# Optimization experiments

Hardware: AMD Instinct MI355X
Metric: run time of the kernel (lower is better)

Reference implementation:

```python
import jax, jax.numpy as jnp
import numpy as np

BS, DEC, IN_LEN, HID, EMB, VOCAB = 16, 100, 512, 768, 768, 32000


def setup_inputs() -> dict:
    key = jax.random.key(0)
    ks = jax.random.split(key, 8)
    x = jax.random.normal(ks[0], (BS, DEC, HID), dtype=jnp.float32)
    attn_dist = jax.random.normal(ks[1], (BS, DEC, IN_LEN), dtype=jnp.float32)
    enc_input = jax.random.randint(ks[2], (BS, IN_LEN), 0, VOCAB, dtype=jnp.int32)
    enc_output = jax.random.normal(ks[3], (BS, IN_LEN, EMB), dtype=jnp.float32)
    # learned params
    W_vocab = jax.random.normal(ks[4], (HID, VOCAB), dtype=jnp.float32) / np.sqrt(HID)
    b_vocab = jnp.zeros((VOCAB,), dtype=jnp.float32)
    W_gen = jax.random.normal(ks[5], (HID + EMB, 1), dtype=jnp.float32) / np.sqrt(HID + EMB)
    b_gen = jnp.zeros((1,), dtype=jnp.float32)
    return {"x": x, "attn_dist": attn_dist, "enc_input": enc_input,
            "enc_output": enc_output, "W_vocab": W_vocab, "b_vocab": b_vocab,
            "W_gen": W_gen, "b_gen": b_gen}


def reference(x, attn_dist, enc_input, enc_output, W_vocab, b_vocab, W_gen, b_gen):
    # context vector: [bs, dec, emb] = attn @ enc_output
    context = jnp.einsum('bdl,ble->bde', attn_dist, enc_output)
    mix = jnp.concatenate([context, x], axis=2)              # [bs, dec, emb+hid]
    p_gen = jax.nn.sigmoid(mix @ W_gen + b_gen)              # [bs, dec, 1]
    logit = x @ W_vocab + b_vocab                            # [bs, dec, vocab]
    vocab_dist = jax.nn.softmax(logit, axis=2) * p_gen       # [bs, dec, vocab]
    attn_w = jax.nn.softmax(attn_dist, axis=2) * (1.0 - p_gen)  # [bs, dec, in_len]
    # scatter_add attention mass onto vocab ids (duplicate ids accumulate)
    b_idx = jnp.arange(BS)[:, None, None]
    d_idx = jnp.arange(DEC)[None, :, None]
    v_idx = enc_input[:, None, :]                            # broadcast over dec
    mixed = vocab_dist.at[b_idx, d_idx, v_idx].add(attn_w)
    return jnp.log(mixed)
```

## Files before the change

### kernel.cpp

```cpp
#include <hip/hip_runtime.h>
#include <math.h>

#define BS 16
#define DEC 100
#define IN_LEN 512
#define HID 768
#define EMB 768
#define VOCAB 32000
#define NROW (BS*DEC)
#define NTILE_M 13
#define NTILE_N2 125
#define KT2 24
#define A_SHORTS 4096
#define B_SHORTS 8192

using short8 = __attribute__((ext_vector_type(8))) short;
using f32x4 = __attribute__((ext_vector_type(4))) float;

__device__ __forceinline__ unsigned short f2bf(float f) {
  unsigned u = __float_as_uint(f);
  u = u + 0x7FFFu + ((u >> 16) & 1u);
  return (unsigned short)(u >> 16);
}
__device__ __forceinline__ float bf2f(unsigned short h) {
  return __uint_as_float(((unsigned)h) << 16);
}

__device__ __forceinline__ void gll16(const void* g, void* l) {
  __builtin_amdgcn_global_load_lds(
      (const __attribute__((address_space(1))) unsigned int*)g,
      (__attribute__((address_space(3))) unsigned int*)l, 16, 0, 0);
}

__global__ __launch_bounds__(256) void k0_venc(const float* __restrict__ enc_out,
                                               const float* __restrict__ Wg,
                                               float* __restrict__ venc) {
  int row = blockIdx.x * 4 + (threadIdx.x >> 6);
  int lane = threadIdx.x & 63;
  const float* p = enc_out + (size_t)row * EMB;
  float s = 0.f;
  for (int e = lane; e < EMB; e += 64) s += p[e] * Wg[e];
  for (int off = 32; off; off >>= 1) s += __shfl_xor(s, off);
  if (lane == 0) venc[row] = s;
}

__global__ __launch_bounds__(256) void k1_row(const float* __restrict__ attn,
                                              const float* __restrict__ x,
                                              const float* __restrict__ venc,
                                              const float* __restrict__ Wg,
                                              const float* __restrict__ bgen,
                                              float* __restrict__ pg,
                                              float* __restrict__ lp,
                                              float* __restrict__ m_a,
                                              float* __restrict__ s_a) {
  int r = blockIdx.x;
  int b = r / DEC;
  int tid = threadIdx.x;
  const float* arow = attn + (size_t)r * IN_LEN;
  const float* ve = venc + b * IN_LEN;
  const float* xrow = x + (size_t)r * HID;

  float pdot = 0.f, m = -1e30f;
  for (int l = tid; l < IN_LEN; l += 256) { float a = arow[l]; pdot += a * ve[l]; m = fmaxf(m, a); }
  for (int h = tid; h < HID; h += 256) pdot += xrow[h] * Wg[HID + h];

  for (int off = 32; off; off >>= 1) pdot += __shfl_xor(pdot, off);
  for (int off = 32; off; off >>= 1) m = fmaxf(m, __shfl_xor(m, off));

  __shared__ float red[8];
  if ((tid & 63) == 0) { red[tid >> 6] = pdot; red[4 + (tid >> 6)] = m; }
  __syncthreads();
  float z = red[0] + red[1] + red[2] + red[3];
  m = fmaxf(fmaxf(red[4], red[5]), fmaxf(red[6], red[7]));

  float se = 0.f;
  for (int l = tid; l < IN_LEN; l += 256) se += expf(arow[l] - m);
  for (int off = 32; off; off >>= 1) se += __shfl_xor(se, off);
  __syncthreads();
  if ((tid & 63) == 0) red[tid >> 6] = se;
  __syncthreads();
  se = red[0] + red[1] + red[2] + red[3];

  if (tid == 0) {
    z += bgen[0];
    float p, l_p;
    if (z >= 0.f) { float e = expf(-z); p = 1.f / (1.f + e); l_p = -log1pf(e); }
    else          { float e = expf(z);  p = e / (1.f + e);   l_p = z - log1pf(e); }
    pg[r] = p; lp[r] = l_p; m_a[r] = m; s_a[r] = se;
  }
}

__global__ __launch_bounds__(256) void p0_pack_x(const float* __restrict__ X,
                                                 unsigned short* __restrict__ Xp) {
  int mtile = blockIdx.x, ks = blockIdx.y, tid = threadIdx.x;
  size_t base = ((size_t)(mtile * KT2 + ks)) * A_SHORTS;
#pragma unroll
  for (int i = 0; i < 2; i++) {
    int u = tid + i * 256;
    int f = u >> 6, l = u & 63;
    int wr = f >> 2, mm = f & 3;
    int row = mtile * 128 + wr * 64 + mm * 16 + (l & 15);
    int k0 = ks * 32 + (l >> 4) * 8;
    short8 v;
    if (row < NROW) {
      const float* p = X + (size_t)row * HID + k0;
#pragma unroll
      for (int j = 0; j < 8; j++) v[j] = (short)f2bf(p[j]);
    } else {
#pragma unroll
      for (int j = 0; j < 8; j++) v[j] = 0;
    }
    *(short8*)&Xp[base + (size_t)u * 8] = v;
  }
}

__global__ __launch_bounds__(256) void p0_pack_w(const float* __restrict__ W,
                                                 unsigned short* __restrict__ Wp) {
  __shared__ float ld[32][257];
  int ntile = blockIdx.x, ks = blockIdx.y, tid = threadIdx.x;
#pragma unroll
  for (int i = 0; i < 32; i++) {
    int idx = tid + i * 256;
    int kk = idx >> 8, nn = idx & 255;
    ld[kk][nn] = W[(size_t)(ks * 32 + kk) * VOCAB + ntile * 256 + nn];
  }
  __syncthreads();
  size_t base = ((size_t)(ntile * KT2 + ks)) * B_SHORTS;
#pragma unroll
  for (int i = 0; i < 4; i++) {
    int u = tid + i * 256;
    int f = u >> 6, l = u & 63;
    int wc, nn;
    if (f < 8) { wc = f >> 2; nn = f & 3; }
    else       { wc = (f - 8) >> 2; nn = 4 + ((f - 8) & 3); }
    int col = wc * 128 + nn * 16 + (l & 15);
    int k0 = (l >> 4) * 8;
    short8 v;
#pragma unroll
    for (int j = 0; j < 8; j++) v[j] = (short)f2bf(ld[k0 + j][col]);
    *(short8*)&Wp[base + (size_t)u * 8] = v;
  }
}

__global__ __launch_bounds__(256, 2) void k2_gemm_v6(const unsigned short* __restrict__ Xp,
                                                     const unsigned short* __restrict__ Wp,
                                                     const float* __restrict__ bvocab,
                                                     float* __restrict__ out,
                                                     unsigned short* __restrict__ lbf,
                                                     float* __restrict__ part,
                                                     int use_bf) {
  __shared__ __align__(16) unsigned short sh[33792];

  int bid = blockIdx.x;
  const int NWG = NTILE_M * NTILE_N2;
  const int q = NWG / 8, rr = NWG % 8;
  int xcd = bid & 7, idx = bid >> 3;
  int wg = (xcd < rr ? xcd * (q + 1) : rr * (q + 1) + (xcd - rr) * q) + idx;
  int ntile = wg / NTILE_M, mtile = wg % NTILE_M;

  const int tid = threadIdx.x;
  const int wid = tid >> 6, lane = tid & 63;
  const int wr = wid >> 1, wc = wid & 1;
  const int l15 = lane & 15, hi = lane >> 4;

  const unsigned short* aSrc = Xp + (size_t)(mtile * KT2) * A_SHORTS;
  const unsigned short* bSrc = Wp + (size_t)(ntile * KT2) * B_SHORTS;
  const unsigned short* bDir = bSrc + (8 + wc * 4) * 512 + lane * 8;

  unsigned short* bufA0 = &sh[0];
  unsigned short* bufA1 = &sh[4096];
  unsigned short* bufB0 = &sh[8192];
  unsigned short* bufB1 = &sh[12288];

  const int aoff = (wr * 4) * 512 + lane * 8;
  const int boff = (wc * 4) * 512 + lane * 8;

  f32x4 acc[4][8] = {};
  short8 af[4], bl[4], rbA[4], rbB[4];

#define STAGE(t, dA, dB) { \
    const unsigned short* a_ = aSrc + (size_t)(t) * A_SHORTS; \
    const unsigned short* b_ = bSrc + (size_t)(t) * B_SHORTS; \
    gll16(a_ + (size_t)tid * 8,         dA + tid * 8); \
    gll16(a_ + (size_t)(tid + 256) * 8, dA + (tid + 256) * 8); \
    gll16(b_ + (size_t)tid * 8,         dB + tid * 8); \
    gll16(b_ + (size_t)(tid + 256) * 8, dB + (tid + 256) * 8); }

#define LOADDIR(dst, t) { \
    const unsigned short* p_ = bDir + (size_t)(t) * B_SHORTS; \
    _Pragma("unroll") for (int nn = 0; nn < 4; nn++) dst[nn] = *(const short8*)(p_ + nn * 512); }

#define DSREAD(bA, bB) { \
    _Pragma("unroll") for (int mm = 0; mm < 4; mm++) af[mm] = *(const short8*)&bA[aoff + mm * 512]; \
    _Pragma("unroll") for (int nn = 0; nn < 4; nn++) bl[nn] = *(const short8*)&bB[boff + nn * 512]; }

#define MFMA32(rb) { \
    _Pragma("unroll") for (int mm = 0; mm < 4; mm++) { \
      _Pragma("unroll") for (int nn = 0; nn < 4; nn++) \
        acc[mm][nn] = __builtin_amdgcn_mfma_f32_16x16x32_bf16(af[mm], bl[nn], acc[mm][nn], 0, 0, 0); \
      _Pragma("unroll") for (int nn = 0; nn < 4; nn++) \
        acc[mm][4 + nn] = __builtin_amdgcn_mfma_f32_16x16x32_bf16(af[mm], rb[nn], acc[mm][4 + nn], 0, 0, 0); } }

  STAGE(0, bufA0, bufB0);
  LOADDIR(rbA, 0);
  asm volatile("s_waitcnt vmcnt(4)" ::: "memory");
  __builtin_amdgcn_s_barrier();
  asm volatile("" ::: "memory");

  for (int tt = 0; tt < 22; tt += 2) {
    STAGE(tt + 1, bufA1, bufB1);
    LOADDIR(rbB, tt + 1);
    DSREAD(bufA0, bufB0);
    __builtin_amdgcn_s_setprio(1);
    MFMA32(rbA);
    __builtin_amdgcn_s_setprio(0);
    asm volatile("s_waitcnt vmcnt(4)" ::: "memory");
    __builtin_amdgcn_s_barrier();
    asm volatile("" ::: "memory");
    STAGE(tt + 2, bufA0, bufB0);
    LOADDIR(rbA, tt + 2);
    DSREAD(bufA1, bufB1);
    __builtin_amdgcn_s_setprio(1);
    MFMA32(rbB);
    __builtin_amdgcn_s_setprio(0);
    asm volatile("s_waitcnt vmcnt(4)" ::: "memory");
    __builtin_amdgcn_s_barrier();
    asm volatile("" ::: "memory");
  }
  STAGE(23, bufA1, bufB1);
  LOADDIR(rbB, 23);
  DSREAD(bufA0, bufB0);
  __builtin_amdgcn_s_setprio(1);
  MFMA32(rbA);
  __builtin_amdgcn_s_setprio(0);
  asm volatile("s_waitcnt vmcnt(4)" ::: "memory");
  __builtin_amdgcn_s_barrier();
  asm volatile("" ::: "memory");
  DSREAD(bufA1, bufB1);
  MFMA32(rbB);
#undef STAGE
#undef LOADDIR
#undef DSREAD
#undef MFMA32

  __syncthreads();

  float bb[8];
#pragma unroll
  for (int nn = 0; nn < 8; nn++) bb[nn] = bvocab[ntile * 256 + wc * 128 + nn * 16 + l15];
#pragma unroll
  for (int mm = 0; mm < 4; mm++)
#pragma unroll
    for (int nn = 0; nn < 8; nn++)
#pragma unroll
      for (int j = 0; j < 4; j++) acc[mm][nn][j] += bb[nn];

  unsigned short* ldsC = &sh[0];
  float* red = (float*)&sh[32768];

  if (use_bf) {
#pragma unroll
    for (int mm = 0; mm < 4; mm++) {
      int row0 = wr * 64 + mm * 16 + hi * 4;
#pragma unroll
      for (int nn = 0; nn < 8; nn++) {
        int col = wc * 128 + nn * 16 + l15;
#pragma unroll
        for (int j = 0; j < 4; j++) ldsC[(row0 + j) * 256 + col] = f2bf(acc[mm][nn][j]);
      }
    }
  } else {
#pragma unroll
    for (int mm = 0; mm < 4; mm++) {
      int row0 = mtile * 128 + wr * 64 + mm * 16 + hi * 4;
#pragma unroll
      for (int nn = 0; nn < 8; nn++) {
        int col = ntile * 256 + wc * 128 + nn * 16 + l15;
#pragma unroll
        for (int j = 0; j < 4; j++) {
          int row = row0 + j;
          if (row < NROW) out[(size_t)row * VOCAB + col] = acc[mm][nn][j];
        }
      }
    }
  }

#pragma unroll
  for (int mm = 0; mm < 4; mm++) {
#pragma unroll
    for (int j = 0; j < 4; j++) {
      float mx = acc[mm][0][j];
#pragma unroll
      for (int nn = 1; nn < 8; nn++) mx = fmaxf(mx, acc[mm][nn][j]);
      mx = fmaxf(mx, __shfl_xor(mx, 1));
      mx = fmaxf(mx, __shfl_xor(mx, 2));
      mx = fmaxf(mx, __shfl_xor(mx, 4));
      mx = fmaxf(mx, __shfl_xor(mx, 8));
      float sl = 0.f;
#pragma unroll
      for (int nn = 0; nn < 8; nn++) sl += __expf(acc[mm][nn][j] - mx);
      sl += __shfl_xor(sl, 1);
      sl += __shfl_xor(sl, 2);
      sl += __shfl_xor(sl, 4);
      sl += __shfl_xor(sl, 8);
      if (l15 == 0) {
        int rloc = wr * 64 + mm * 16 + hi * 4 + j;
        int o = (rloc * 2 + wc) * 2;
        red[o] = mx; red[o + 1] = sl;
      }
    }
  }
  __syncthreads();

  if (use_bf) {
#pragma unroll
    for (int i = 0; i < 16; i++) {
      int flat = tid + i * 256;
      int r = flat >> 5, c = (flat & 31) * 8;
      int grow = mtile * 128 + r;
      if (grow < NROW)
        *(short8*)&lbf[(size_t)grow * VOCAB + ntile * 256 + c] = *(const short8*)&ldsC[r * 256 + c];
    }
  }
  if (tid < 128) {
    int o0 = (tid * 2 + 0) * 2;
    int o1 = (tid * 2 + 1) * 2;
    float m0 = red[o0], s0 = red[o0 + 1];
    float m1 = red[o1], s1 = red[o1 + 1];
    float m = fmaxf(m0, m1);
    float s = s0 * __expf(m0 - m) + s1 * __expf(m1 - m);
    int grow = mtile * 128 + tid;
    if (grow < NROW) {
      part[(size_t)grow * 256 + ntile * 2]     = m;
      part[(size_t)grow * 256 + ntile * 2 + 1] = s;
    }
  }
}

__global__ __launch_bounds__(512) void k4_fused(float* __restrict__ out,
                                                const unsigned short* __restrict__ lbf,
                                                const float* __restrict__ part,
                                                const float* __restrict__ lp,
                                                const float* __restrict__ attn,
                                                const int* __restrict__ enc,
                                                const float* __restrict__ pg,
                                                const float* __restrict__ m_a,
                                                const float* __restrict__ s_a) {
  int r = blockIdx.x >> 1;
  int half = blockIdx.x & 1;
  int tid = threadIdx.x;
  __shared__ float sm[8], ss[8], sc[1];
  __shared__ int   s_key[1024];
  __shared__ float s_val[1024];
  s_key[tid] = -1; s_key[tid + 512] = -1;
  s_val[tid] = 0.f; s_val[tid + 512] = 0.f;

  float m = -1e30f, s = 0.f;
  if (tid < NTILE_N2) {
    m = part[(size_t)r * 256 + tid * 2];
    s = part[(size_t)r * 256 + tid * 2 + 1];
  }
  for (int off = 1; off < 64; off <<= 1) {
    float mo = __shfl_xor(m, off), so = __shfl_xor(s, off);
    float nm = fmaxf(m, mo);
    s = s * __expf(m - nm) + so * __expf(mo - nm);
    m = nm;
  }
  if ((tid & 63) == 0) { sm[tid >> 6] = m; ss[tid >> 6] = s; }
  __syncthreads();
  if (tid == 0) {
    float mm_ = sm[0], ss_ = ss[0];
    for (int w = 1; w < 8; w++) {
      float nm = fmaxf(mm_, sm[w]);
      ss_ = ss_ * __expf(mm_ - nm) + ss[w] * __expf(sm[w] - nm);
      mm_ = nm;
    }
    sc[0] = lp[r] - (mm_ + __logf(ss_));
  }

  float omp = 1.f - pg[r];
  if (omp > 0.f) {
    int b_ = r / DEC;
    float t = omp * __expf(attn[(size_t)r * IN_LEN + tid] - m_a[r]) / s_a[r];
    int v = enc[b_ * IN_LEN + tid];
    int slot = v & 1023;
    while (true) {
      int old = atomicCAS(&s_key[slot], -1, v);
      if (old == -1 || old == v) { atomicAdd(&s_val[slot], t); break; }
      slot = (slot + 1) & 1023;
    }
  }
  __syncthreads();
  float coef = sc[0];

  const int HUNITS = (VOCAB / 8) / 2;
  const short8* src = (const short8*)(lbf + (size_t)r * VOCAB) + (size_t)half * HUNITS;
  float* dst = out + (size_t)r * VOCAB;
  float* dsth = dst + (size_t)half * (VOCAB / 2);
  for (int i = tid; i < HUNITS; i += 512) {
    short8 v = src[i];
    f32x4 a, b;
    a[0] = bf2f((unsigned short)v[0]) + coef; a[1] = bf2f((unsigned short)v[1]) + coef;
    a[2] = bf2f((unsigned short)v[2]) + coef; a[3] = bf2f((unsigned short)v[3]) + coef;
    b[0] = bf2f((unsigned short)v[4]) + coef; b[1] = bf2f((unsigned short)v[5]) + coef;
    b[2] = bf2f((unsigned short)v[6]) + coef; b[3] = bf2f((unsigned short)v[7]) + coef;
    __builtin_nontemporal_store(a, (f32x4*)&dsth[i * 8]);
    __builtin_nontemporal_store(b, (f32x4*)&dsth[i * 8 + 4]);
  }
  __syncthreads();

  int lo = half * (VOCAB / 2), hiR = lo + (VOCAB / 2);
  for (int i = tid; i < 1024; i += 512) {
    int v = s_key[i];
    if (v >= lo && v < hiR) {
      float sum = s_val[i];
      float p = dst[v];
      dst[v] = logf(expf(p) + sum);
    }
  }
}

__global__ __launch_bounds__(256) void k4_finish(float* __restrict__ out,
                                                 const float* __restrict__ part,
                                                 const float* __restrict__ lp) {
  int r = blockIdx.x >> 1, half = blockIdx.x & 1;
  int tid = threadIdx.x;
  float m = -1e30f, s = 0.f;
  if (tid < NTILE_N2) {
    m = part[(size_t)r * 256 + tid * 2];
    s = part[(size_t)r * 256 + tid * 2 + 1];
  }
  for (int off = 1; off < 64; off <<= 1) {
    float mo = __shfl_xor(m, off), so = __shfl_xor(s, off);
    float nm = fmaxf(m, mo);
    s = s * __expf(m - nm) + so * __expf(mo - nm);
    m = nm;
  }
  __shared__ float sm[4], ss[4], sc[1];
  if ((tid & 63) == 0) { sm[tid >> 6] = m; ss[tid >> 6] = s; }
  __syncthreads();
  if (tid == 0) {
    float mm_ = sm[0], ss_ = ss[0];
    for (int w = 1; w < 4; w++) {
      float nm = fmaxf(mm_, sm[w]);
      ss_ = ss_ * __expf(mm_ - nm) + ss[w] * __expf(sm[w] - nm);
      mm_ = nm;
    }
    sc[0] = lp[r] - (mm_ + __logf(ss_));
  }
  __syncthreads();
  float coef = sc[0];
  float4* p = (float4*)(out + (size_t)r * VOCAB + half * (VOCAB / 2));
  for (int i = tid; i < VOCAB / 8; i += 256) {
    float4 v = p[i];
    v.x += coef; v.y += coef; v.z += coef; v.w += coef;
    p[i] = v;
  }
}

__global__ __launch_bounds__(256) void k4_scatter(float* __restrict__ out,
                                                  const float* __restrict__ attn,
                                                  const int* __restrict__ enc,
                                                  const float* __restrict__ pg,
                                                  const float* __restrict__ m_a,
                                                  const float* __restrict__ s_a) {
  int idx = blockIdx.x * 256 + threadIdx.x;
  int l = idx & (IN_LEN - 1);
  int r = idx >> 9;
  int b = r / DEC;
  float omp = 1.f - pg[r];
  if (omp <= 0.f) return;
  float term = omp * expf(attn[(size_t)r * IN_LEN + l] - m_a[r]) / s_a[r];
  int v = enc[b * IN_LEN + l];
  unsigned* ua = (unsigned*)(out + (size_t)r * VOCAB + v);
  unsigned old = *ua;
  while (true) {
    float f = __uint_as_float(old);
    float nf = logf(expf(f) + term);
    unsigned assumed = old;
    old = atomicCAS(ua, assumed, __float_as_uint(nf));
    if (old == assumed) break;
  }
}

#define BM 128
#define BN 128
#define BK 32
__device__ __forceinline__ int swz_old(int row, int k) {
  int slot = (k >> 3) ^ ((row >> 1) & 3);
  return row * 32 + slot * 8 + (k & 7);
}

__global__ __launch_bounds__(256) void k2_gemm_old(const float* __restrict__ X,
                                                   const float* __restrict__ W,
                                                   const float* __restrict__ bvocab,
                                                   float* __restrict__ out) {
  __shared__ __align__(16) unsigned short As[BM * BK];
  __shared__ __align__(16) unsigned short Bs[BN * BK];
  const int mtile = blockIdx.x;
  const int ntile = blockIdx.y;
  const int tid = threadIdx.x;
  const int wid = tid >> 6, lane = tid & 63;
  const int wr = wid >> 1, wc = wid & 1;
  f32x4 acc[4][4] = {};
  float4 areg[4];
  float  breg[16];
  const int nl = tid & 127;
  const int kg = tid >> 7;
  {
#pragma unroll
    for (int i = 0; i < 4; i++) {
      int idx = tid + i * 256;
      int r = mtile * BM + (idx >> 3);
      if (r < NROW) areg[i] = *(const float4*)(X + (size_t)r * HID + (idx & 7) * 4);
      else areg[i] = make_float4(0.f, 0.f, 0.f, 0.f);
    }
    const float* base = W + (size_t)(kg * 16) * VOCAB + ntile * BN + nl;
#pragma unroll
    for (int i = 0; i < 16; i++) breg[i] = base[(size_t)i * VOCAB];
  }
  const int KS = HID / BK;
  for (int ks = 0; ks < KS; ++ks) {
#pragma unroll
    for (int i = 0; i < 4; i++) {
      int idx = tid + i * 256;
      int r = idx >> 3, kq = idx & 7;
      unsigned short w0 = f2bf(areg[i].x), w1 = f2bf(areg[i].y);
      unsigned short w2 = f2bf(areg[i].z), w3 = f2bf(areg[i].w);
      unsigned short* dstp = &As[swz_old(r, kq * 4)];
      dstp[0] = w0; dstp[1] = w1; dstp[2] = w2; dstp[3] = w3;
    }
    {
      short8 v0, v1;
#pragma unroll
      for (int i = 0; i < 8; i++) { v0[i] = (short)f2bf(breg[i]); v1[i] = (short)f2bf(breg[8 + i]); }
      *(short8*)&Bs[swz_old(nl, kg * 16)] = v0;
      *(short8*)&Bs[swz_old(nl, kg * 16 + 8)] = v1;
    }
    __syncthreads();
    if (ks + 1 < KS) {
      const int ksn = ks + 1;
#pragma unroll
      for (int i = 0; i < 4; i++) {
        int idx = tid + i * 256;
        int r = mtile * BM + (idx >> 3);
        if (r < NROW) areg[i] = *(const float4*)(X + (size_t)r * HID + ksn * BK + (idx & 7) * 4);
        else areg[i] = make_float4(0.f, 0.f, 0.f, 0.f);
      }
      const float* base = W + (size_t)(ksn * BK + kg * 16) * VOCAB + ntile * BN + nl;
#pragma unroll
      for (int i = 0; i < 16; i++) breg[i] = base[(size_t)i * VOCAB];
    }
    {
      const int k0 = (lane >> 4) * 8;
      const int rbase = wr * 64 + (lane & 15);
      const int cbase = wc * 64 + (lane & 15);
      short8 af[4], bf[4];
#pragma unroll
      for (int mm = 0; mm < 4; mm++) af[mm] = *(const short8*)&As[swz_old(rbase + mm * 16, k0)];
#pragma unroll
      for (int nn = 0; nn < 4; nn++) bf[nn] = *(const short8*)&Bs[swz_old(cbase + nn * 16, k0)];
#pragma unroll
      for (int mm = 0; mm < 4; mm++)
#pragma unroll
        for (int nn = 0; nn < 4; nn++)
          acc[mm][nn] = __builtin_amdgcn_mfma_f32_16x16x32_bf16(af[mm], bf[nn], acc[mm][nn], 0, 0, 0);
    }
    __syncthreads();
  }
#pragma unroll
  for (int mm = 0; mm < 4; mm++) {
    int row0 = mtile * BM + wr * 64 + mm * 16 + (lane >> 4) * 4;
#pragma unroll
    for (int nn = 0; nn < 4; nn++) {
      int col = ntile * BN + wc * 64 + nn * 16 + (lane & 15);
      float bb = bvocab[col];
#pragma unroll
      for (int j = 0; j < 4; j++) {
        int row = row0 + j;
        if (row < NROW) out[(size_t)row * VOCAB + col] = acc[mm][nn][j] + bb;
      }
    }
  }
}

__global__ __launch_bounds__(256) void k3_norm(float* __restrict__ out,
                                               const float* __restrict__ lp) {
  int r = blockIdx.x;
  float4* row = reinterpret_cast<float4*>(out + (size_t)r * VOCAB);
  int tid = threadIdx.x;
  float m = -1e30f, s = 0.f;
  for (int i = tid; i < VOCAB / 4; i += 256) {
    float4 v = row[i];
    float m4 = fmaxf(fmaxf(v.x, v.y), fmaxf(v.z, v.w));
    if (m4 > m) { s *= __expf(m - m4); m = m4; }
    s += __expf(v.x - m) + __expf(v.y - m) + __expf(v.z - m) + __expf(v.w - m);
  }
  for (int off = 32; off; off >>= 1) {
    float mo = __shfl_xor(m, off), so = __shfl_xor(s, off);
    float nm = fmaxf(m, mo);
    s = s * __expf(m - nm) + so * __expf(mo - nm);
    m = nm;
  }
  __shared__ float mred[4], sred[4];
  if ((tid & 63) == 0) { mred[tid >> 6] = m; sred[tid >> 6] = s; }
  __syncthreads();
  if (tid == 0) {
    float mm = mred[0], ss = sred[0];
    for (int w = 1; w < 4; w++) {
      float mo = mred[w], so = sred[w];
      float nm = fmaxf(mm, mo);
      ss = ss * __expf(mm - nm) + so * __expf(mo - nm);
      mm = nm;
    }
    mred[0] = mm; sred[0] = ss;
  }
  __syncthreads();
  m = mred[0]; s = sred[0];
  float coef = lp[r] - (m + __logf(s));
  for (int i = tid; i < VOCAB / 4; i += 256) {
    float4 v = row[i];
    v.x += coef; v.y += coef; v.z += coef; v.w += coef;
    row[i] = v;
  }
}

extern "C" void kernel_launch(void* const* d_in, const int* in_sizes, int n_in,
                              void* d_out, int out_size, void* d_ws, size_t ws_size,
                              hipStream_t stream) {
  (void)in_sizes; (void)n_in; (void)out_size;
  const float* x       = (const float*)d_in[0];
  const float* attn    = (const float*)d_in[1];
  const int*   enc_in  = (const int*)d_in[2];
  const float* enc_out = (const float*)d_in[3];
  const float* Wv      = (const float*)d_in[4];
  const float* bv      = (const float*)d_in[5];
  const float* Wg      = (const float*)d_in[6];
  const float* bg      = (const float*)d_in[7];
  float* out = (float*)d_out;
  float* ws  = (float*)d_ws;

  float* venc = ws;
  float* pg   = ws + 8192;
  float* lp   = ws + 9792;
  float* m_a  = ws + 11392;
  float* s_a  = ws + 12992;
  float* part = ws + 14592;
  unsigned short* Xp = (unsigned short*)(ws + 814592);
  unsigned short* Wp = (unsigned short*)(ws + 1453568);
  unsigned short* Lbf = (unsigned short*)(ws + 13741568);
  const size_t NEED  = (size_t)13741568 * 4;
  const size_t NEED2 = NEED + (size_t)NROW * VOCAB * 2;

  hipLaunchKernelGGL(k0_venc, dim3(2048), dim3(256), 0, stream, enc_out, Wg, venc);
  hipLaunchKernelGGL(k1_row, dim3(NROW), dim3(256), 0, stream, attn, x, venc, Wg, bg,
                     pg, lp, m_a, s_a);

  if (ws_size >= NEED) {
    int use_bf = (ws_size >= NEED2) ? 1 : 0;
    hipLaunchKernelGGL(p0_pack_x, dim3(NTILE_M, KT2), dim3(256), 0, stream, x, Xp);
    hipLaunchKernelGGL(p0_pack_w, dim3(NTILE_N2, KT2), dim3(256), 0, stream, Wv, Wp);
    hipLaunchKernelGGL(k2_gemm_v6, dim3(NTILE_M * NTILE_N2), dim3(256), 0, stream,
                       Xp, Wp, bv, out, Lbf, part, use_bf);
    if (use_bf) {
      hipLaunchKernelGGL(k4_fused, dim3(NROW * 2), dim3(512), 0, stream,
                         out, Lbf, part, lp, attn, enc_in, pg, m_a, s_a);
    } else {
      hipLaunchKernelGGL(k4_finish, dim3(NROW * 2), dim3(256), 0, stream, out, part, lp);
      hipLaunchKernelGGL(k4_scatter, dim3((NROW * IN_LEN) / 256), dim3(256), 0, stream,
                         out, attn, enc_in, pg, m_a, s_a);
    }
  } else {
    hipLaunchKernelGGL(k2_gemm_old, dim3(NTILE_M, 250), dim3(256), 0, stream,
                       x, Wv, bv, out);
    hipLaunchKernelGGL(k3_norm, dim3(NROW), dim3(256), 0, stream, out, lp);
    hipLaunchKernelGGL(k4_scatter, dim3((NROW * IN_LEN) / 256), dim3(256), 0, stream,
                       out, attn, enc_in, pg, m_a, s_a);
  }
}
```

Measured before the change: 239.9 us.

## Enlarge GEMM tile to 256x256 with 8 waves and triple-buffered LDS

```diff
diff --git a/kernel.cpp b/kernel.cpp
--- a/kernel.cpp
+++ b/kernel.cpp
@@ -8,11 +8,12 @@
 #define EMB 768
 #define VOCAB 32000
 #define NROW (BS*DEC)
-#define NTILE_M 13
+#define NTILE_M3 7
 #define NTILE_N2 125
 #define KT2 24
-#define A_SHORTS 4096
+#define A3_SHORTS 8192
 #define B_SHORTS 8192
+#define BUF_SHORTS 16384
 
 using short8 = __attribute__((ext_vector_type(8))) short;
 using f32x4 = __attribute__((ext_vector_type(4))) float;
@@ -93,13 +94,13 @@
 __global__ __launch_bounds__(256) void p0_pack_x(const float* __restrict__ X,
                                                  unsigned short* __restrict__ Xp) {
   int mtile = blockIdx.x, ks = blockIdx.y, tid = threadIdx.x;
-  size_t base = ((size_t)(mtile * KT2 + ks)) * A_SHORTS;
-#pragma unroll
-  for (int i = 0; i < 2; i++) {
+  size_t base = ((size_t)(mtile * KT2 + ks)) * A3_SHORTS;
+#pragma unroll
+  for (int i = 0; i < 4; i++) {
     int u = tid + i * 256;
     int f = u >> 6, l = u & 63;
     int wr = f >> 2, mm = f & 3;
-    int row = mtile * 128 + wr * 64 + mm * 16 + (l & 15);
+    int row = mtile * 256 + wr * 64 + mm * 16 + (l & 15);
     int k0 = ks * 32 + (l >> 4) * 8;
     short8 v;
     if (row < NROW) {
@@ -130,9 +131,7 @@
   for (int i = 0; i < 4; i++) {
     int u = tid + i * 256;
     int f = u >> 6, l = u & 63;
-    int wc, nn;
-    if (f < 8) { wc = f >> 2; nn = f & 3; }
-    else       { wc = (f - 8) >> 2; nn = 4 + ((f - 8) & 3); }
+    int wc = f >> 3, nn = f & 7;
     int col = wc * 128 + nn * 16 + (l & 15);
     int k0 = (l >> 4) * 8;
     short8 v;
@@ -142,104 +141,80 @@
   }
 }
 
-__global__ __launch_bounds__(256, 2) void k2_gemm_v6(const unsigned short* __restrict__ Xp,
+__global__ __launch_bounds__(512, 2) void k2_gemm_v7(const unsigned short* __restrict__ Xp,
                                                      const unsigned short* __restrict__ Wp,
                                                      const float* __restrict__ bvocab,
                                                      float* __restrict__ out,
                                                      unsigned short* __restrict__ lbf,
                                                      float* __restrict__ part,
                                                      int use_bf) {
-  __shared__ __align__(16) unsigned short sh[33792];
+  __shared__ __align__(16) unsigned short sh[3 * BUF_SHORTS];
+  __shared__ float red[1024];
 
   int bid = blockIdx.x;
-  const int NWG = NTILE_M * NTILE_N2;
+  const int NWG = NTILE_M3 * NTILE_N2;
   const int q = NWG / 8, rr = NWG % 8;
   int xcd = bid & 7, idx = bid >> 3;
   int wg = (xcd < rr ? xcd * (q + 1) : rr * (q + 1) + (xcd - rr) * q) + idx;
-  int ntile = wg / NTILE_M, mtile = wg % NTILE_M;
+  int ntile = wg / NTILE_M3, mtile = wg % NTILE_M3;
 
   const int tid = threadIdx.x;
   const int wid = tid >> 6, lane = tid & 63;
   const int wr = wid >> 1, wc = wid & 1;
   const int l15 = lane & 15, hi = lane >> 4;
 
-  const unsigned short* aSrc = Xp + (size_t)(mtile * KT2) * A_SHORTS;
+  const unsigned short* aSrc = Xp + (size_t)(mtile * KT2) * A3_SHORTS;
   const unsigned short* bSrc = Wp + (size_t)(ntile * KT2) * B_SHORTS;
-  const unsigned short* bDir = bSrc + (8 + wc * 4) * 512 + lane * 8;
-
-  unsigned short* bufA0 = &sh[0];
-  unsigned short* bufA1 = &sh[4096];
-  unsigned short* bufB0 = &sh[8192];
-  unsigned short* bufB1 = &sh[12288];
 
   const int aoff = (wr * 4) * 512 + lane * 8;
-  const int boff = (wc * 4) * 512 + lane * 8;
+  const int boff = (wc * 8) * 512 + lane * 8;
 
   f32x4 acc[4][8] = {};
-  short8 af[4], bl[4], rbA[4], rbB[4];
-
-#define STAGE(t, dA, dB) { \
-    const unsigned short* a_ = aSrc + (size_t)(t) * A_SHORTS; \
+  short8 af[4], bl[8];
+
+#define STAGE(t, bufidx) { \
+    const unsigned short* a_ = aSrc + (size_t)(t) * A3_SHORTS; \
     const unsigned short* b_ = bSrc + (size_t)(t) * B_SHORTS; \
-    gll16(a_ + (size_t)tid * 8,         dA + tid * 8); \
-    gll16(a_ + (size_t)(tid + 256) * 8, dA + (tid + 256) * 8); \
-    gll16(b_ + (size_t)tid * 8,         dB + tid * 8); \
-    gll16(b_ + (size_t)(tid + 256) * 8, dB + (tid + 256) * 8); }
-
-#define LOADDIR(dst, t) { \
-    const unsigned short* p_ = bDir + (size_t)(t) * B_SHORTS; \
-    _Pragma("unroll") for (int nn = 0; nn < 4; nn++) dst[nn] = *(const short8*)(p_ + nn * 512); }
-
-#define DSREAD(bA, bB) { \
-    _Pragma("unroll") for (int mm = 0; mm < 4; mm++) af[mm] = *(const short8*)&bA[aoff + mm * 512]; \
-    _Pragma("unroll") for (int nn = 0; nn < 4; nn++) bl[nn] = *(const short8*)&bB[boff + nn * 512]; }
-
-#define MFMA32(rb) { \
-    _Pragma("unroll") for (int mm = 0; mm < 4; mm++) { \
-      _Pragma("unroll") for (int nn = 0; nn < 4; nn++) \
-        acc[mm][nn] = __builtin_amdgcn_mfma_f32_16x16x32_bf16(af[mm], bl[nn], acc[mm][nn], 0, 0, 0); \
-      _Pragma("unroll") for (int nn = 0; nn < 4; nn++) \
-        acc[mm][4 + nn] = __builtin_amdgcn_mfma_f32_16x16x32_bf16(af[mm], rb[nn], acc[mm][4 + nn], 0, 0, 0); } }
-
-  STAGE(0, bufA0, bufB0);
-  LOADDIR(rbA, 0);
+    unsigned short* d_ = &sh[(bufidx) * BUF_SHORTS]; \
+    gll16(a_ + (size_t)tid * 8,         d_ + tid * 8); \
+    gll16(a_ + (size_t)(tid + 512) * 8, d_ + (tid + 512) * 8); \
+    gll16(b_ + (size_t)tid * 8,         d_ + 8192 + tid * 8); \
+    gll16(b_ + (size_t)(tid + 512) * 8, d_ + 8192 + (tid + 512) * 8); }
+
+#define DSREAD(bufidx) { \
+    const unsigned short* A_ = &sh[(bufidx) * BUF_SHORTS]; \
+    const unsigned short* B_ = A_ + 8192; \
+    _Pragma("unroll") for (int mm = 0; mm < 4; mm++) af[mm] = *(const short8*)&A_[aoff + mm * 512]; \
+    _Pragma("unroll") for (int nn = 0; nn < 8; nn++) bl[nn] = *(const short8*)&B_[boff + nn * 512]; }
+
+#define MFMA32() { \
+    _Pragma("unroll") for (int mm = 0; mm < 4; mm++) \
+    _Pragma("unroll") for (int nn = 0; nn < 8; nn++) \
+      acc[mm][nn] = __builtin_amdgcn_mfma_f32_16x16x32_bf16(af[mm], bl[nn], acc[mm][nn], 0, 0, 0); }
+
+  STAGE(0, 0);
+  STAGE(1, 1);
   asm volatile("s_waitcnt vmcnt(4)" ::: "memory");
   __builtin_amdgcn_s_barrier();
   asm volatile("" ::: "memory");
 
-  for (int tt = 0; tt < 22; tt += 2) {
-    STAGE(tt + 1, bufA1, bufB1);
-    LOADDIR(rbB, tt + 1);
-    DSREAD(bufA0, bufB0);
+  int bcur = 0;
+  for (int t = 0; t < KT2; ++t) {
+    if (t + 2 < KT2) {
+      int bn = bcur + 2; if (bn >= 3) bn -= 3;
+      STAGE(t + 2, bn);
+    }
+    DSREAD(bcur);
     __builtin_amdgcn_s_setprio(1);
-    MFMA32(rbA);
+    MFMA32();
     __builtin_amdgcn_s_setprio(0);
-    asm volatile("s_waitcnt vmcnt(4)" ::: "memory");
+    if (t < KT2 - 2) { asm volatile("s_waitcnt vmcnt(4)" ::: "memory"); }
+    else             { asm volatile("s_waitcnt vmcnt(0)" ::: "memory"); }
     __builtin_amdgcn_s_barrier();
     asm volatile("" ::: "memory");
-    STAGE(tt + 2, bufA0, bufB0);
-    LOADDIR(rbA, tt + 2);
-    DSREAD(bufA1, bufB1);
-    __builtin_amdgcn_s_setprio(1);
-    MFMA32(rbB);
-    __builtin_amdgcn_s_setprio(0);
-    asm volatile("s_waitcnt vmcnt(4)" ::: "memory");
-    __builtin_amdgcn_s_barrier();
-    asm volatile("" ::: "memory");
-  }
-  STAGE(23, bufA1, bufB1);
-  LOADDIR(rbB, 23);
-  DSREAD(bufA0, bufB0);
-  __builtin_amdgcn_s_setprio(1);
-  MFMA32(rbA);
-  __builtin_amdgcn_s_setprio(0);
-  asm volatile("s_waitcnt vmcnt(4)" ::: "memory");
-  __builtin_amdgcn_s_barrier();
-  asm volatile("" ::: "memory");
-  DSREAD(bufA1, bufB1);
-  MFMA32(rbB);
+    bcur = bcur + 1; if (bcur >= 3) bcur = 0;
+  }
 #undef STAGE
-#undef LOADDIR
 #undef DSREAD
 #undef MFMA32
 
@@ -254,36 +229,6 @@
     for (int nn = 0; nn < 8; nn++)
 #pragma unroll
       for (int j = 0; j < 4; j++) acc[mm][nn][j] += bb[nn];
-
-  unsigned short* ldsC = &sh[0];
-  float* red = (float*)&sh[32768];
-
-  if (use_bf) {
-#pragma unroll
-    for (int mm = 0; mm < 4; mm++) {
-      int row0 = wr * 64 + mm * 16 + hi * 4;
-#pragma unroll
-      for (int nn = 0; nn < 8; nn++) {
-        int col = wc * 128 + nn * 16 + l15;
-#pragma unroll
-        for (int j = 0; j < 4; j++) ldsC[(row0 + j) * 256 + col] = f2bf(acc[mm][nn][j]);
-      }
-    }
-  } else {
-#pragma unroll
-    for (int mm = 0; mm < 4; mm++) {
-      int row0 = mtile * 128 + wr * 64 + mm * 16 + hi * 4;
-#pragma unroll
-      for (int nn = 0; nn < 8; nn++) {
-        int col = ntile * 256 + wc * 128 + nn * 16 + l15;
-#pragma unroll
-        for (int j = 0; j < 4; j++) {
-          int row = row0 + j;
-          if (row < NROW) out[(size_t)row * VOCAB + col] = acc[mm][nn][j];
-        }
-      }
-    }
-  }
 
 #pragma unroll
   for (int mm = 0; mm < 4; mm++) {
@@ -305,34 +250,68 @@
       sl += __shfl_xor(sl, 8);
       if (l15 == 0) {
         int rloc = wr * 64 + mm * 16 + hi * 4 + j;
-        int o = (rloc * 2 + wc) * 2;
-        red[o] = mx; red[o + 1] = sl;
+        red[(rloc * 2 + wc) * 2]     = mx;
+        red[(rloc * 2 + wc) * 2 + 1] = sl;
       }
     }
   }
   __syncthreads();
 
-  if (use_bf) {
-#pragma unroll
-    for (int i = 0; i < 16; i++) {
-      int flat = tid + i * 256;
-      int r = flat >> 5, c = (flat & 31) * 8;
-      int grow = mtile * 128 + r;
-      if (grow < NROW)
-        *(short8*)&lbf[(size_t)grow * VOCAB + ntile * 256 + c] = *(const short8*)&ldsC[r * 256 + c];
-    }
-  }
-  if (tid < 128) {
+  if (tid < 256) {
     int o0 = (tid * 2 + 0) * 2;
     int o1 = (tid * 2 + 1) * 2;
     float m0 = red[o0], s0 = red[o0 + 1];
     float m1 = red[o1], s1 = red[o1 + 1];
     float m = fmaxf(m0, m1);
     float s = s0 * __expf(m0 - m) + s1 * __expf(m1 - m);
-    int grow = mtile * 128 + tid;
+    int grow = mtile * 256 + tid;
     if (grow < NROW) {
       part[(size_t)grow * 256 + ntile * 2]     = m;
       part[(size_t)grow * 256 + ntile * 2 + 1] = s;
+    }
+  }
+
+  unsigned short* ldsC = &sh[0];
+  if (use_bf) {
+#pragma unroll
+    for (int h = 0; h < 2; h++) {
+      if ((wr >> 1) == h) {
+        int rl0 = (wr & 1) * 64;
+#pragma unroll
+        for (int mm = 0; mm < 4; mm++) {
+          int row0 = rl0 + mm * 16 + hi * 4;
+#pragma unroll
+          for (int nn = 0; nn < 8; nn++) {
+            int col = wc * 128 + nn * 16 + l15;
+#pragma unroll
+            for (int j = 0; j < 4; j++) ldsC[(row0 + j) * 256 + col] = f2bf(acc[mm][nn][j]);
+          }
+        }
+      }
+      __syncthreads();
+#pragma unroll
+      for (int i = 0; i < 8; i++) {
+        int flat = tid + i * 512;
+        int r = flat >> 5, c = (flat & 31) * 8;
+        int grow = mtile * 256 + h * 128 + r;
+        if (grow < NROW)
+          *(short8*)&lbf[(size_t)grow * VOCAB + ntile * 256 + c] = *(const short8*)&ldsC[r * 256 + c];
+      }
+      __syncthreads();
+    }
+  } else {
+#pragma unroll
+    for (int mm = 0; mm < 4; mm++) {
+      int row0 = mtile * 256 + wr * 64 + mm * 16 + hi * 4;
+#pragma unroll
+      for (int nn = 0; nn < 8; nn++) {
+        int col = ntile * 256 + wc * 128 + nn * 16 + l15;
+#pragma unroll
+        for (int j = 0; j < 4; j++) {
+          int row = row0 + j;
+          if (row < NROW) out[(size_t)row * VOCAB + col] = acc[mm][nn][j];
+        }
+      }
     }
   }
 }
@@ -647,9 +626,9 @@
   float* s_a  = ws + 12992;
   float* part = ws + 14592;
   unsigned short* Xp = (unsigned short*)(ws + 814592);
-  unsigned short* Wp = (unsigned short*)(ws + 1453568);
-  unsigned short* Lbf = (unsigned short*)(ws + 13741568);
-  const size_t NEED  = (size_t)13741568 * 4;
+  unsigned short* Wp = (unsigned short*)(ws + 1502720);
+  unsigned short* Lbf = (unsigned short*)(ws + 13790720);
+  const size_t NEED  = (size_t)13790720 * 4;
   const size_t NEED2 = NEED + (size_t)NROW * VOCAB * 2;
 
   hipLaunchKernelGGL(k0_venc, dim3(2048), dim3(256), 0, stream, enc_out, Wg, venc);
@@ -658,9 +637,9 @@
 
   if (ws_size >= NEED) {
     int use_bf = (ws_size >= NEED2) ? 1 : 0;
-    hipLaunchKernelGGL(p0_pack_x, dim3(NTILE_M, KT2), dim3(256), 0, stream, x, Xp);
+    hipLaunchKernelGGL(p0_pack_x, dim3(NTILE_M3, KT2), dim3(256), 0, stream, x, Xp);
     hipLaunchKernelGGL(p0_pack_w, dim3(NTILE_N2, KT2), dim3(256), 0, stream, Wv, Wp);
-    hipLaunchKernelGGL(k2_gemm_v6, dim3(NTILE_M * NTILE_N2), dim3(256), 0, stream,
+    hipLaunchKernelGGL(k2_gemm_v7, dim3(NTILE_M3 * NTILE_N2), dim3(512), 0, stream,
                        Xp, Wp, bv, out, Lbf, part, use_bf);
     if (use_bf) {
       hipLaunchKernelGGL(k4_fused, dim3(NROW * 2), dim3(512), 0, stream,
@@ -671,7 +650,7 @@
                          out, attn, enc_in, pg, m_a, s_a);
     }
   } else {
-    hipLaunchKernelGGL(k2_gemm_old, dim3(NTILE_M, 250), dim3(256), 0, stream,
+    hipLaunchKernelGGL(k2_gemm_old, dim3(13, 250), dim3(256), 0, stream,
                        x, Wv, bv, out);
     hipLaunchKernelGGL(k3_norm, dim3(NROW), dim3(256), 0, stream, out, lp);
     hipLaunchKernelGGL(k4_scatter, dim3((NROW * IN_LEN) / 256), dim3(256), 0, stream,
```

New measurement: 284.2 us. 18.5% more time.

## Triple-buffer GEMM LDS staging and shrink epilogue staging to half-tile passes

Applied to the files above, without the earlier changes.

```diff
diff --git a/kernel.cpp b/kernel.cpp
--- a/kernel.cpp
+++ b/kernel.cpp
@@ -142,14 +142,14 @@
   }
 }
 
-__global__ __launch_bounds__(256, 2) void k2_gemm_v6(const unsigned short* __restrict__ Xp,
+__global__ __launch_bounds__(256, 2) void k2_gemm_v8(const unsigned short* __restrict__ Xp,
                                                      const unsigned short* __restrict__ Wp,
                                                      const float* __restrict__ bvocab,
                                                      float* __restrict__ out,
                                                      unsigned short* __restrict__ lbf,
                                                      float* __restrict__ part,
                                                      int use_bf) {
-  __shared__ __align__(16) unsigned short sh[33792];
+  __shared__ __align__(16) unsigned short sh[25600];
 
   int bid = blockIdx.x;
   const int NWG = NTILE_M * NTILE_N2;
@@ -167,32 +167,30 @@
   const unsigned short* bSrc = Wp + (size_t)(ntile * KT2) * B_SHORTS;
   const unsigned short* bDir = bSrc + (8 + wc * 4) * 512 + lane * 8;
 
-  unsigned short* bufA0 = &sh[0];
-  unsigned short* bufA1 = &sh[4096];
-  unsigned short* bufB0 = &sh[8192];
-  unsigned short* bufB1 = &sh[12288];
-
   const int aoff = (wr * 4) * 512 + lane * 8;
   const int boff = (wc * 4) * 512 + lane * 8;
 
   f32x4 acc[4][8] = {};
   short8 af[4], bl[4], rbA[4], rbB[4];
 
-#define STAGE(t, dA, dB) { \
+#define STAGE(t, bufidx) { \
     const unsigned short* a_ = aSrc + (size_t)(t) * A_SHORTS; \
     const unsigned short* b_ = bSrc + (size_t)(t) * B_SHORTS; \
-    gll16(a_ + (size_t)tid * 8,         dA + tid * 8); \
-    gll16(a_ + (size_t)(tid + 256) * 8, dA + (tid + 256) * 8); \
-    gll16(b_ + (size_t)tid * 8,         dB + tid * 8); \
-    gll16(b_ + (size_t)(tid + 256) * 8, dB + (tid + 256) * 8); }
+    unsigned short* d_ = &sh[(bufidx) * 8192]; \
+    gll16(a_ + (size_t)tid * 8,          d_ + tid * 8); \
+    gll16(a_ + (size_t)(tid + 256) * 8,  d_ + (tid + 256) * 8); \
+    gll16(b_ + (size_t)tid * 8,          d_ + 4096 + tid * 8); \
+    gll16(b_ + (size_t)(tid + 256) * 8,  d_ + 4096 + (tid + 256) * 8); }
 
 #define LOADDIR(dst, t) { \
     const unsigned short* p_ = bDir + (size_t)(t) * B_SHORTS; \
     _Pragma("unroll") for (int nn = 0; nn < 4; nn++) dst[nn] = *(const short8*)(p_ + nn * 512); }
 
-#define DSREAD(bA, bB) { \
-    _Pragma("unroll") for (int mm = 0; mm < 4; mm++) af[mm] = *(const short8*)&bA[aoff + mm * 512]; \
-    _Pragma("unroll") for (int nn = 0; nn < 4; nn++) bl[nn] = *(const short8*)&bB[boff + nn * 512]; }
+#define DSREAD(bufidx) { \
+    const unsigned short* A_ = &sh[(bufidx) * 8192]; \
+    const unsigned short* B_ = A_ + 4096; \
+    _Pragma("unroll") for (int mm = 0; mm < 4; mm++) af[mm] = *(const short8*)&A_[aoff + mm * 512]; \
+    _Pragma("unroll") for (int nn = 0; nn < 4; nn++) bl[nn] = *(const short8*)&B_[boff + nn * 512]; }
 
 #define MFMA32(rb) { \
     _Pragma("unroll") for (int mm = 0; mm < 4; mm++) { \
@@ -201,43 +199,46 @@
       _Pragma("unroll") for (int nn = 0; nn < 4; nn++) \
         acc[mm][4 + nn] = __builtin_amdgcn_mfma_f32_16x16x32_bf16(af[mm], rb[nn], acc[mm][4 + nn], 0, 0, 0); } }
 
-  STAGE(0, bufA0, bufB0);
+  STAGE(0, 0);
+  STAGE(1, 1);
   LOADDIR(rbA, 0);
-  asm volatile("s_waitcnt vmcnt(4)" ::: "memory");
+  asm volatile("s_waitcnt vmcnt(8)" ::: "memory");
   __builtin_amdgcn_s_barrier();
   asm volatile("" ::: "memory");
 
-  for (int tt = 0; tt < 22; tt += 2) {
-    STAGE(tt + 1, bufA1, bufB1);
-    LOADDIR(rbB, tt + 1);
-    DSREAD(bufA0, bufB0);
-    __builtin_amdgcn_s_setprio(1);
-    MFMA32(rbA);
-    __builtin_amdgcn_s_setprio(0);
-    asm volatile("s_waitcnt vmcnt(4)" ::: "memory");
-    __builtin_amdgcn_s_barrier();
-    asm volatile("" ::: "memory");
-    STAGE(tt + 2, bufA0, bufB0);
-    LOADDIR(rbA, tt + 2);
-    DSREAD(bufA1, bufB1);
-    __builtin_amdgcn_s_setprio(1);
-    MFMA32(rbB);
-    __builtin_amdgcn_s_setprio(0);
-    asm volatile("s_waitcnt vmcnt(4)" ::: "memory");
-    __builtin_amdgcn_s_barrier();
-    asm volatile("" ::: "memory");
-  }
-  STAGE(23, bufA1, bufB1);
-  LOADDIR(rbB, 23);
-  DSREAD(bufA0, bufB0);
-  __builtin_amdgcn_s_setprio(1);
-  MFMA32(rbA);
-  __builtin_amdgcn_s_setprio(0);
-  asm volatile("s_waitcnt vmcnt(4)" ::: "memory");
-  __builtin_amdgcn_s_barrier();
-  asm volatile("" ::: "memory");
-  DSREAD(bufA1, bufB1);
-  MFMA32(rbB);
+  int bcur = 0;
+  for (int tt = 0; tt < KT2; tt += 2) {
+    {
+      int t = tt;
+      int bn = bcur + 2; if (bn >= 3) bn -= 3;
+      if (t + 2 < KT2) STAGE(t + 2, bn);
+      if (t + 1 < KT2) LOADDIR(rbB, t + 1);
+      DSREAD(bcur);
+      __builtin_amdgcn_s_setprio(1);
+      MFMA32(rbA);
+      __builtin_amdgcn_s_setprio(0);
+      if (t < KT2 - 2) { asm volatile("s_waitcnt vmcnt(8)" ::: "memory"); }
+      else             { asm volatile("s_waitcnt vmcnt(0)" ::: "memory"); }
+      __builtin_amdgcn_s_barrier();
+      asm volatile("" ::: "memory");
+      bcur = bcur + 1; if (bcur >= 3) bcur = 0;
+    }
+    {
+      int t = tt + 1;
+      int bn = bcur + 2; if (bn >= 3) bn -= 3;
+      if (t + 2 < KT2) STAGE(t + 2, bn);
+      if (t + 1 < KT2) LOADDIR(rbA, t + 1);
+      DSREAD(bcur);
+      __builtin_amdgcn_s_setprio(1);
+      MFMA32(rbB);
+      __builtin_amdgcn_s_setprio(0);
+      if (t < KT2 - 2) { asm volatile("s_waitcnt vmcnt(8)" ::: "memory"); }
+      else             { asm volatile("s_waitcnt vmcnt(0)" ::: "memory"); }
+      __builtin_amdgcn_s_barrier();
+      asm volatile("" ::: "memory");
+      bcur = bcur + 1; if (bcur >= 3) bcur = 0;
+    }
+  }
 #undef STAGE
 #undef LOADDIR
 #undef DSREAD
@@ -255,35 +256,7 @@
 #pragma unroll
       for (int j = 0; j < 4; j++) acc[mm][nn][j] += bb[nn];
 
-  unsigned short* ldsC = &sh[0];
-  float* red = (float*)&sh[32768];
-
-  if (use_bf) {
-#pragma unroll
-    for (int mm = 0; mm < 4; mm++) {
-      int row0 = wr * 64 + mm * 16 + hi * 4;
-#pragma unroll
-      for (int nn = 0; nn < 8; nn++) {
-        int col = wc * 128 + nn * 16 + l15;
-#pragma unroll
-        for (int j = 0; j < 4; j++) ldsC[(row0 + j) * 256 + col] = f2bf(acc[mm][nn][j]);
-      }
-    }
-  } else {
-#pragma unroll
-    for (int mm = 0; mm < 4; mm++) {
-      int row0 = mtile * 128 + wr * 64 + mm * 16 + hi * 4;
-#pragma unroll
-      for (int nn = 0; nn < 8; nn++) {
-        int col = ntile * 256 + wc * 128 + nn * 16 + l15;
-#pragma unroll
-        for (int j = 0; j < 4; j++) {
-          int row = row0 + j;
-          if (row < NROW) out[(size_t)row * VOCAB + col] = acc[mm][nn][j];
-        }
-      }
-    }
-  }
+  float* red = (float*)&sh[24576];
 
 #pragma unroll
   for (int mm = 0; mm < 4; mm++) {
@@ -312,16 +285,6 @@
   }
   __syncthreads();
 
-  if (use_bf) {
-#pragma unroll
-    for (int i = 0; i < 16; i++) {
-      int flat = tid + i * 256;
-      int r = flat >> 5, c = (flat & 31) * 8;
-      int grow = mtile * 128 + r;
-      if (grow < NROW)
-        *(short8*)&lbf[(size_t)grow * VOCAB + ntile * 256 + c] = *(const short8*)&ldsC[r * 256 + c];
-    }
-  }
   if (tid < 128) {
     int o0 = (tid * 2 + 0) * 2;
     int o1 = (tid * 2 + 1) * 2;
@@ -333,6 +296,50 @@
     if (grow < NROW) {
       part[(size_t)grow * 256 + ntile * 2]     = m;
       part[(size_t)grow * 256 + ntile * 2 + 1] = s;
+    }
+  }
+
+  if (use_bf) {
+    unsigned short* ldsC = &sh[0];
+#pragma unroll
+    for (int p = 0; p < 2; p++) {
+      if (wc == p) {
+#pragma unroll
+        for (int mm = 0; mm < 4; mm++) {
+          int row0 = wr * 64 + mm * 16 + hi * 4;
+#pragma unroll
+          for (int nn = 0; nn < 8; nn++) {
+            int coll = nn * 16 + l15;
+#pragma unroll
+            for (int j = 0; j < 4; j++) ldsC[(row0 + j) * 128 + coll] = f2bf(acc[mm][nn][j]);
+          }
+        }
+      }
+      __syncthreads();
+#pragma unroll
+      for (int i = 0; i < 8; i++) {
+        int flat = tid + i * 256;
+        int r = flat >> 4, c = (flat & 15) * 8;
+        int grow = mtile * 128 + r;
+        if (grow < NROW)
+          *(short8*)&lbf[(size_t)grow * VOCAB + ntile * 256 + p * 128 + c] =
+              *(const short8*)&ldsC[r * 128 + c];
+      }
+      __syncthreads();
+    }
+  } else {
+#pragma unroll
+    for (int mm = 0; mm < 4; mm++) {
+      int row0 = mtile * 128 + wr * 64 + mm * 16 + hi * 4;
+#pragma unroll
+      for (int nn = 0; nn < 8; nn++) {
+        int col = ntile * 256 + wc * 128 + nn * 16 + l15;
+#pragma unroll
+        for (int j = 0; j < 4; j++) {
+          int row = row0 + j;
+          if (row < NROW) out[(size_t)row * VOCAB + col] = acc[mm][nn][j];
+        }
+      }
     }
   }
 }
@@ -660,7 +667,7 @@
     int use_bf = (ws_size >= NEED2) ? 1 : 0;
     hipLaunchKernelGGL(p0_pack_x, dim3(NTILE_M, KT2), dim3(256), 0, stream, x, Xp);
     hipLaunchKernelGGL(p0_pack_w, dim3(NTILE_N2, KT2), dim3(256), 0, stream, Wv, Wp);
-    hipLaunchKernelGGL(k2_gemm_v6, dim3(NTILE_M * NTILE_N2), dim3(256), 0, stream,
+    hipLaunchKernelGGL(k2_gemm_v8, dim3(NTILE_M * NTILE_N2), dim3(256), 0, stream,
                        Xp, Wp, bv, out, Lbf, part, use_bf);
     if (use_bf) {
       hipLaunchKernelGGL(k4_fused, dim3(NROW * 2), dim3(512), 0, stream,
@@ -671,7 +678,7 @@
                          out, attn, enc_in, pg, m_a, s_a);
     }
   } else {
-    hipLaunchKernelGGL(k2_gemm_old, dim3(NTILE_M, 250), dim3(256), 0, stream,
+    hipLaunchKernelGGL(k2_gemm_old, dim3(13, 250), dim3(256), 0, stream,
                        x, Wv, bv, out);
     hipLaunchKernelGGL(k3_norm, dim3(NROW), dim3(256), 0, stream, out, lp);
     hipLaunchKernelGGL(k4_scatter, dim3((NROW * IN_LEN) / 256), dim3(256), 0, stream,
```

Result: slower. 248.5 us (+3.6%).
